# Kernel tuning notes

Measured on AMD Instinct MI355X. Metric: run time of the kernel, lower is better.

## Reference

```python
import jax, jax.numpy as jnp
import numpy as np

NUM_CLASSES = 15
ANGLE_BINS = 90
ANGLE_SCALE = float(np.pi / 2 / ANGLE_BINS)
TOPK, A_ALPHA, A_BETA = 13, 1.0, 6.0
F_ALPHA, F_GAMMA = 0.75, 2.0
W_CLS, W_BOX, W_ANGLE = 1.0, 2.5, 0.05
EPS = 1e-9


def make_anchors(img=1024, strides=(8, 16, 32)):
    pts, strs = [], []
    for s in strides:
        n = img // s
        xs = (np.arange(n, dtype=np.float32) + 0.5) * s  # pixel-space centers
        X, Y = np.meshgrid(xs, xs)
        pts.append(np.stack([X.ravel(), Y.ravel()], -1))
        strs.append(np.full((n * n, 1), s, np.float32))
    return np.concatenate(pts)[None].astype(np.float32), np.concatenate(strs)[None]


def decode_boxes(anchor_points, reg_dist, raw_angles, stride_tensor, angle_proj):
    # DFL-style angle: softmax over bins projected onto angle values
    angle = jnp.einsum('bna,a->bn', jax.nn.softmax(raw_angles, axis=-1), angle_proj)  # [B,N]
    lt, rb = reg_dist[..., :2], reg_dist[..., 2:]
    off = (rb - lt) * 0.5
    c, s = jnp.cos(angle), jnp.sin(angle)
    ox = off[..., 0] * c - off[..., 1] * s
    oy = off[..., 0] * s + off[..., 1] * c
    xy = jnp.stack([ox, oy], -1) * stride_tensor + anchor_points
    wh = (lt + rb) * stride_tensor
    return jnp.concatenate([xy, wh, angle[..., None]], -1)  # [B,N,5]


def _cov(b):
    # rotated box -> 2D Gaussian covariance terms
    w, h, a = b[..., 2], b[..., 3], b[..., 4]
    A, B = w * w / 12.0, h * h / 12.0
    c, s = jnp.cos(a), jnp.sin(a)
    return A * c * c + B * s * s, A * s * s + B * c * c, (A - B) * c * s


def probiou_hd(b1, b2, eps=1e-3):
    # Hellinger distance between Gaussian boxes; probiou similarity = 1 - hd
    x1, y1, x2, y2 = b1[..., 0], b1[..., 1], b2[..., 0], b2[..., 1]
    a1, bb1, c1 = _cov(b1)
    a2, bb2, c2 = _cov(b2)
    denom = (a1 + a2) * (bb1 + bb2) - (c1 + c2) ** 2 + eps
    t1 = ((a1 + a2) * (y1 - y2) ** 2 + (bb1 + bb2) * (x1 - x2) ** 2) / denom * 0.25
    t2 = ((c1 + c2) * (x2 - x1) * (y1 - y2)) / denom * 0.5
    det1 = jnp.maximum(a1 * bb1 - c1 * c1, 0.0)
    det2 = jnp.maximum(a2 * bb2 - c2 * c2, 0.0)
    t3 = 0.5 * jnp.log(denom / (4.0 * jnp.sqrt(det1 * det2) + eps) + eps)
    bd = jnp.clip(t1 + t2 + t3, eps, 100.0)
    return jnp.sqrt(1.0 - jnp.exp(-bd) + 1e-7)


def assign(pred_scores, pred_boxes, anchor_points, gt_labels, gt_boxes, pad_gt_mask, bg_index):
    B, M = gt_labels.shape[:2]
    N = pred_boxes.shape[1]
    C = pred_scores.shape[-1]
    lbl = gt_labels[..., 0]  # [B,M]
    # rotated ProbIoU between every GT and every pred box: [B,M,N]
    ious = jnp.maximum(1.0 - probiou_hd(gt_boxes[:, :, None, :], pred_boxes[:, None, :, :]), 0.0)
    # gather pred class score at each gt's label: [B,M,N]
    scores = jnp.einsum('bnc,bmc->bmn', pred_scores, jax.nn.one_hot(lbl, C, dtype=pred_scores.dtype))
    align = (scores ** A_ALPHA) * (ious ** A_BETA)
    # anchor-center inside rotated GT box
    dx = anchor_points[:, None, :, 0] - gt_boxes[:, :, None, 0]
    dy = anchor_points[:, None, :, 1] - gt_boxes[:, :, None, 1]
    ca, sa = jnp.cos(gt_boxes[:, :, None, 4]), jnp.sin(gt_boxes[:, :, None, 4])
    xr = dx * ca + dy * sa
    yr = -dx * sa + dy * ca
    in_gt = (jnp.abs(xr) < gt_boxes[:, :, None, 2] * 0.5) & (jnp.abs(yr) < gt_boxes[:, :, None, 3] * 0.5)
    mask_cand = in_gt.astype(align.dtype) * pad_gt_mask  # [B,M,N]
    # top-k alignment candidates per GT
    topv, topi = jax.lax.top_k(align * mask_cand, TOPK)
    valid = (topv > EPS).astype(align.dtype)
    bi = jnp.arange(B)[:, None, None]
    mi = jnp.arange(M)[None, :, None]
    topk_mask = jnp.zeros((B, M, N), align.dtype).at[bi, mi, topi].max(valid)
    mask_pos = topk_mask * mask_cand
    # resolve anchors matched to multiple GTs via max IoU
    fg = mask_pos.sum(1)  # [B,N]
    is_max_iou = jax.nn.one_hot(jnp.argmax(ious, axis=1), M, axis=1, dtype=align.dtype)
    mask_pos = jnp.where(fg[:, None, :] > 1, is_max_iou, mask_pos)
    fg = mask_pos.sum(1)
    tgt_idx = jnp.argmax(mask_pos, axis=1)  # [B,N]
    fg_mask = fg > 0
    assigned_labels = jnp.where(fg_mask, jnp.take_along_axis(lbl, tgt_idx, axis=1), bg_index)
    assigned_boxes = jnp.take_along_axis(gt_boxes, tgt_idx[..., None], axis=1)  # [B,N,5]
    # normalize alignment metric by per-GT max IoU / max align
    align_pos = align * mask_pos
    max_align = align_pos.max(-1, keepdims=True)
    max_iou = (ious * mask_pos).max(-1, keepdims=True)
    norm_align = (align_pos * max_iou / (max_align + EPS)).max(1)  # [B,N]
    onehot = jax.nn.one_hot(assigned_labels, C + 1, dtype=align.dtype)[..., :C]
    assigned_scores = onehot * norm_align[..., None]
    return assigned_labels, assigned_boxes, assigned_scores


def _bce_logits(x, t):
    return jnp.maximum(x, 0.0) - x * t + jnp.log1p(jnp.exp(-jnp.abs(x)))


def compute_loss(cls_logits, reg_dist, raw_angles, gt_labels, gt_boxes, valid_mask,
                 anchor_points, stride_tensor, angle_proj):
    C = NUM_CLASSES
    decoded = decode_boxes(anchor_points, reg_dist, raw_angles, stride_tensor, angle_proj)
    cls_scores = jax.nn.sigmoid(cls_logits)
    al, ab, ascore = assign(jax.lax.stop_gradient(cls_scores), jax.lax.stop_gradient(decoded),
                            anchor_points, gt_labels, gt_boxes, valid_mask, C)
    score_sum = jnp.maximum(ascore.sum(), 1.0)
    # varifocal classification loss
    onehot = jax.nn.one_hot(al, C + 1, dtype=cls_logits.dtype)[..., :C]
    fw = F_ALPHA * (cls_scores ** F_GAMMA) * (1.0 - onehot) + ascore * onehot
    loss_cls = (_bce_logits(cls_logits, ascore) * fw).sum() / score_sum
    # ProbIoU box loss over positives, weighted by assigned scores
    posf = (al != C).astype(cls_logits.dtype)
    iou_loss = probiou_hd(decoded, ab)  # [B,N]
    bw = ascore.sum(-1)
    loss_box = (iou_loss * bw * posf).sum() / score_sum
    # DFL angle loss: interpolate CE between neighboring bins
    t = jnp.clip(ab[..., 4] / ANGLE_SCALE, 0.0, ANGLE_BINS - 0.01)
    li = t.astype(jnp.int32)
    ri = jnp.minimum(li + 1, ANGLE_BINS)
    lw = ri.astype(t.dtype) - t
    rw = 1.0 - lw
    logp = jax.nn.log_softmax(raw_angles, axis=-1)
    ce_l = -jnp.take_along_axis(logp, li[..., None], axis=-1)[..., 0]
    ce_r = -jnp.take_along_axis(logp, ri[..., None], axis=-1)[..., 0]
    npos = jnp.maximum(posf.sum(), 1.0)
    loss_angle = ((ce_l * lw + ce_r * rw) * posf).sum() / npos
    total = W_CLS * loss_cls + W_BOX * loss_box + W_ANGLE * loss_angle
    return total, loss_cls, loss_box, loss_angle


def setup_inputs() -> dict:
    key = jax.random.key(0)
    ks = jax.random.split(key, 8)
    B, M, C, AB = 16, 64, NUM_CLASSES, ANGLE_BINS
    anchor_np, stride_np = make_anchors()
    N = anchor_np.shape[1]  # 21504
    cls_logits = jax.random.normal(ks[0], (B, N, C), jnp.float32) - 2.0
    reg_dist = jax.random.uniform(ks[1], (B, N, 4), jnp.float32, 0.0, 6.0)
    raw_angles = jax.random.normal(ks[2], (B, N, AB + 1), jnp.float32)
    gt_labels = jax.random.randint(ks[3], (B, M, 1), 0, C)
    cxy = jax.random.uniform(ks[4], (B, M, 2), jnp.float32, 32.0, 992.0)
    wh = jax.random.uniform(ks[5], (B, M, 2), jnp.float32, 16.0, 160.0)
    ang = jax.random.uniform(ks[6], (B, M, 1), jnp.float32, 0.0, float(np.pi / 2) - 1e-3)
    gt_boxes = jnp.concatenate([cxy, wh, ang], -1)
    valid_mask = (jax.random.uniform(ks[7], (B, M, 1)) < 0.8).astype(jnp.float32)
    angle_proj = jnp.arange(AB + 1, dtype=jnp.float32) * ANGLE_SCALE
    return dict(cls_logits=cls_logits, reg_dist=reg_dist, raw_angles=raw_angles,
                gt_labels=gt_labels, gt_boxes=gt_boxes, valid_mask=valid_mask,
                anchor_points=jnp.asarray(anchor_np), stride_tensor=jnp.asarray(stride_np),
                angle_proj=angle_proj)


def reference(cls_logits, reg_dist, raw_angles, gt_labels, gt_boxes, valid_mask,
              anchor_points, stride_tensor, angle_proj):
    return compute_loss(cls_logits, reg_dist, raw_angles, gt_labels, gt_boxes, valid_mask,
                        anchor_points, stride_tensor, angle_proj)
```

## Files before the change

kernel.cpp:

```cpp
#include <hip/hip_runtime.h>

#define TK 13
#define EPSA 1e-9f
#define MMAX 128
#define CMAX 1024
#define DROWS 64
#define A1F 91
#define CF 15

__device__ __forceinline__ float frcp(float x) { return __builtin_amdgcn_rcpf(x); }

__device__ __forceinline__ void anchor_of(int n, float& ax, float& ay, float& st) {
    if (n < 16384)      { st = 8.0f;  ax = ((n & 127) + 0.5f) * 8.0f;  ay = ((n >> 7) + 0.5f) * 8.0f; }
    else if (n < 20480) { int q = n - 16384; st = 16.0f; ax = ((q & 63) + 0.5f) * 16.0f; ay = ((q >> 6) + 0.5f) * 16.0f; }
    else                { int q = n - 20480; st = 32.0f; ax = ((q & 31) + 0.5f) * 32.0f; ay = ((q >> 5) + 0.5f) * 32.0f; }
}

__device__ __forceinline__ float hd_cov(float x1, float y1, float a1, float b1, float c1, float sd1,
                                        float x2, float y2, float a2, float b2, float c2, float sd2) {
    float sa = a1 + a2, sb = b1 + b2, sc = c1 + c2;
    float denom = sa * sb - sc * sc + 1e-3f;
    float inv = frcp(denom);
    float dy = y1 - y2, dx = x1 - x2;
    float t1 = (sa * dy * dy + sb * dx * dx) * inv * 0.25f;
    float t2 = sc * (x2 - x1) * (y1 - y2) * inv * 0.5f;
    float t3 = 0.5f * __logf(denom * frcp(4.0f * sd1 * sd2 + 1e-3f) + 1e-3f);
    float bd = fminf(fmaxf(t1 + t2 + t3, 1e-3f), 100.0f);
    return sqrtf(1.0f - __expf(-bd) + 1e-7f);
}

__device__ __forceinline__ void cov5(float w, float h, float ang,
                                     float& ca, float& cb, float& cc, float& sd) {
    float A = w * w * (1.0f / 12.0f), B = h * h * (1.0f / 12.0f);
    float c = __cosf(ang), s = __sinf(ang);
    ca = A * c * c + B * s * s;
    cb = A * s * s + B * c * c;
    cc = (A - B) * c * s;
    sd = sqrtf(fmaxf(ca * cb - cc * cc, 0.0f));
}

__global__ __launch_bounds__(256) void k_decode(
    const float* __restrict__ reg, const float* __restrict__ rawang,
    float4* __restrict__ dec4, float2* __restrict__ dcs,
    float* __restrict__ lse_out,
    int* __restrict__ zbase, int zwords,
    int BN, int N) {
    __shared__ float srow[DROWS * A1F];
    int tid = threadIdx.x;
    int gstride = gridDim.x * 256;
    for (int z = blockIdx.x * 256 + tid; z < zwords; z += gstride) zbase[z] = 0;
    int r0 = blockIdx.x * DROWS;
    if (r0 >= BN) return;
    if (r0 + DROWS <= BN) {
        const float4* g4 = (const float4*)(rawang + (size_t)r0 * A1F);
        float4* s4 = (float4*)srow;
#pragma unroll
        for (int k = 0; k < (DROWS * A1F) / 4 / 256 + 1; ++k) {
            int j = tid + k * 256;
            if (j < (DROWS * A1F) / 4) s4[j] = g4[j];
        }
    } else {
        const float* gs = rawang + (size_t)r0 * A1F;
        int lim = (BN - r0) * A1F;
        for (int k = tid; k < lim; k += 256) srow[k] = gs[k];
    }
    __syncthreads();
    int row = tid >> 2, sub = tid & 3;
    int idx = r0 + row;
    if (idx >= BN) return;
    int j0 = sub * 23;
    int jn = (sub == 3) ? 22 : 23;
    const float* rp = srow + row * A1F + j0;
    float s = 0.0f, num = 0.0f;
#pragma unroll
    for (int i = 0; i < 23; ++i) {
        if (i < jn) {
            float e = __expf(rp[i]);
            s += e;
            num = fmaf(e, (float)(j0 + i), num);
        }
    }
    s += __shfl_xor(s, 1); num += __shfl_xor(num, 1);
    s += __shfl_xor(s, 2); num += __shfl_xor(num, 2);
    if (sub == 0) {
        float ang = 0.017453292519943295f * num * frcp(s);
        float lse = __logf(s);
        int n = idx % N;
        float4 rg = *(const float4*)(reg + (size_t)idx * 4);
        float l0 = rg.x, l1 = rg.y, rr0 = rg.z, rr1 = rg.w;
        float offx = (rr0 - l0) * 0.5f, offy = (rr1 - l1) * 0.5f;
        float c = __cosf(ang), sn = __sinf(ang);
        float ox = offx * c - offy * sn, oy = offx * sn + offy * c;
        float ax, ay, st;
        anchor_of(n, ax, ay, st);
        float x = ox * st + ax;
        float y = oy * st + ay;
        float w = (l0 + rr0) * st, hh = (l1 + rr1) * st;
        float ca, cb, cc, sd;
        cov5(w, hh, ang, ca, cb, cc, sd);
        dec4[idx] = make_float4(x, y, ca, cb);
        dcs[idx] = make_float2(cc, sd);
        lse_out[idx] = lse;
    }
}

__global__ __launch_bounds__(256) void k_topk(
    const float4* __restrict__ dec4, const float2* __restrict__ dcs,
    const float* __restrict__ cls,
    const float* __restrict__ gtb, const int* __restrict__ gtl,
    const float* __restrict__ vmask,
    int* __restrict__ fg, int* __restrict__ tgtc,
    int B, int M, int N, int C) {
    int m = blockIdx.x, b = blockIdx.y;
    if (vmask[b * M + m] == 0.0f) return;
    const float* g = gtb + (size_t)(b * M + m) * 5;
    float gx = g[0], gy = g[1], gw = g[2], gh = g[3], gang = g[4];
    float gca, gcb, gcc, gsd;
    cov5(gw, gh, gang, gca, gcb, gcc, gsd);
    float cA = __cosf(gang), sA = __sinf(gang);
    int lbl = gtl[b * M + m];
    float hw = 0.5f * gw, hh2 = 0.5f * gh;
    float hx = fabsf(hw * cA) + fabsf(hh2 * sA);
    float hy = fabsf(hw * sA) + fabsf(hh2 * cA);
    int tid = threadIdx.x;
    size_t bN = (size_t)b * N;

    __shared__ int cnt;
    __shared__ float cval[CMAX];
    __shared__ int cidx[CMAX];
    if (tid == 0) cnt = 0;
    __syncthreads();

    const int off_[3] = {0, 16384, 20480};
    const int gs_[3]  = {128, 64, 32};
    const float st_[3] = {8.0f, 16.0f, 32.0f};
#pragma unroll
    for (int lv = 0; lv < 3; ++lv) {
        float st = st_[lv];
        int gs = gs_[lv], off = off_[lv];
        float ist = frcp(st);
        int i0 = (int)floorf((gx - hx) * ist - 0.5f);
        int i1 = (int)ceilf((gx + hx) * ist - 0.5f);
        int j0 = (int)floorf((gy - hy) * ist - 0.5f);
        int j1 = (int)ceilf((gy + hy) * ist - 0.5f);
        i0 = max(i0, 0); j0 = max(j0, 0);
        i1 = min(i1, gs - 1); j1 = min(j1, gs - 1);
        int w = i1 - i0 + 1, hgt = j1 - j0 + 1;
        int tot = (w > 0 && hgt > 0) ? w * hgt : 0;
        for (int t = tid; t < tot; t += 256) {
            int ii = i0 + t % w, jj = j0 + t / w;
            float ax = (ii + 0.5f) * st, ay = (jj + 0.5f) * st;
            float dx = ax - gx, dy = ay - gy;
            float xr = dx * cA + dy * sA;
            float yr = -dx * sA + dy * cA;
            if (fabsf(xr) < hw && fabsf(yr) < hh2) {
                int n = off + jj * gs + ii;
                float4 dd = dec4[bN + n];
                float2 cs = dcs[bN + n];
                float hd = hd_cov(gx, gy, gca, gcb, gcc, gsd,
                                  dd.x, dd.y, dd.z, dd.w, cs.x, cs.y);
                float iou = fmaxf(1.0f - hd, 0.0f);
                float xl = cls[(bN + n) * C + lbl];
                float p = frcp(1.0f + __expf(-xl));
                float i2 = iou * iou;
                float v = p * (i2 * i2 * i2);
                if (v > EPSA) {
                    int pos = atomicAdd(&cnt, 1);
                    if (pos < CMAX) { cval[pos] = v; cidx[pos] = n; }
                }
            }
        }
    }
    __syncthreads();

    int total = min(cnt, CMAX);
    int rounds = min(total, TK);
    if (tid < 64) {
        for (int r = 0; r < rounds; ++r) {
            float bv = -1.0f; int bn = 0x7fffffff; int bp = -1;
            for (int j = tid; j < total; j += 64) {
                float v = cval[j];
                int nn = cidx[j];
                if (v > bv || (v == bv && nn < bn)) { bv = v; bn = nn; bp = j; }
            }
            for (int o = 32; o; o >>= 1) {
                float ov = __shfl_xor(bv, o);
                int on = __shfl_xor(bn, o);
                int op = __shfl_xor(bp, o);
                if (ov > bv || (ov == bv && on < bn)) { bv = ov; bn = on; bp = op; }
            }
            if (tid == 0) {
                atomicAdd(&fg[bN + bn], 1);
                atomicMax(&tgtc[bN + bn], m);
            }
            if ((bp & 63) == tid) cval[bp] = -2.0f;
        }
    }
}

__global__ __launch_bounds__(256) void k_select(
    const float4* __restrict__ dec4, const float2* __restrict__ dcs,
    const float* __restrict__ cls,
    const float* __restrict__ gtb, const int* __restrict__ gtl,
    const int* __restrict__ fg, const int* __restrict__ tgtc,
    int* __restrict__ tgt_out, float* __restrict__ align_out,
    unsigned int* __restrict__ max_align, unsigned int* __restrict__ max_iou,
    int B, int M, int N, int C) {
    __shared__ float gx[MMAX], gy[MMAX], ga[MMAX], gb[MMAX], gc[MMAX], gsd[MMAX];
    __shared__ int glb[MMAX];
    int b = blockIdx.y;
    int tid = threadIdx.x;
    if (tid < M) {
        const float* g = gtb + (size_t)(b * M + tid) * 5;
        float ca, cb, cc, sd;
        cov5(g[2], g[3], g[4], ca, cb, cc, sd);
        gx[tid] = g[0]; gy[tid] = g[1]; ga[tid] = ca; gb[tid] = cb; gc[tid] = cc; gsd[tid] = sd;
        glb[tid] = gtl[b * M + tid];
    }
    __syncthreads();
    int n = blockIdx.x * 256 + tid;
    if (n >= N) return;
    size_t bN = (size_t)b * N;
    int f = fg[bN + n];
    if (f == 0) return;
    float4 dd = dec4[bN + n];
    float2 cs = dcs[bN + n];
    float px = dd.x, py = dd.y, pa = dd.z, pb = dd.w, pc = cs.x, psd = cs.y;
    int mstar;
    float ioustar;
    if (f == 1) {
        mstar = tgtc[bN + n];
        float hd = hd_cov(gx[mstar], gy[mstar], ga[mstar], gb[mstar], gc[mstar], gsd[mstar],
                          px, py, pa, pb, pc, psd);
        ioustar = fmaxf(1.0f - hd, 0.0f);
    } else {
        float best = -1.0f; int bm = 0;
        for (int mm = 0; mm < M; mm++) {
            float hd = hd_cov(gx[mm], gy[mm], ga[mm], gb[mm], gc[mm], gsd[mm],
                              px, py, pa, pb, pc, psd);
            float iou = fmaxf(1.0f - hd, 0.0f);
            if (iou > best) { best = iou; bm = mm; }
        }
        mstar = bm; ioustar = best;
    }
    int lbl = glb[mstar];
    float xl = cls[(bN + n) * C + lbl];
    float p = frcp(1.0f + __expf(-xl));
    float i2 = ioustar * ioustar;
    float al = p * (i2 * i2 * i2);
    tgt_out[bN + n] = mstar + 1;
    align_out[bN + n] = al;
    atomicMax(&max_align[b * M + mstar], __float_as_uint(al));
    atomicMax(&max_iou[b * M + mstar], __float_as_uint(ioustar));
}

__global__ __launch_bounds__(256) void k_loss(
    const float4* __restrict__ dec4, const float2* __restrict__ dcs,
    const float* __restrict__ cls,
    const float* __restrict__ rawang, const float* __restrict__ lse_in,
    const float* __restrict__ gtb, const int* __restrict__ gtl,
    const int* __restrict__ tgt_in, const float* __restrict__ align_in,
    const float* __restrict__ max_align, const float* __restrict__ max_iou,
    float* __restrict__ pblk,
    int B, int M, int N, int C, int A1) {
    __shared__ float gx[MMAX], gy[MMAX], ga[MMAX], gb[MMAX], gc[MMAX], gsd[MMAX], gan[MMAX];
    __shared__ int glb[MMAX];
    int b = blockIdx.y;
    int tid = threadIdx.x;
    if (tid < M) {
        const float* g = gtb + (size_t)(b * M + tid) * 5;
        float ca, cb, cc, sd;
        cov5(g[2], g[3], g[4], ca, cb, cc, sd);
        gx[tid] = g[0]; gy[tid] = g[1]; ga[tid] = ca; gb[tid] = cb; gc[tid] = cc; gsd[tid] = sd;
        gan[tid] = g[4];
        glb[tid] = gtl[b * M + tid];
    }
    __syncthreads();
    int n = blockIdx.x * 256 + tid;
    float s_cls = 0.0f, s_box = 0.0f, s_ang = 0.0f, s_asc = 0.0f, s_pos = 0.0f;
    if (n < N) {
        size_t bN = (size_t)b * N;
        int tg1 = tgt_in[bN + n];
        int lbl = -1;
        float norm = 0.0f;
        if (tg1 > 0) {
            int tg = tg1 - 1;
            lbl = glb[tg];
            norm = align_in[bN + n] * max_iou[b * M + tg] * frcp(max_align[b * M + tg] + 1e-9f);
            float4 dd = dec4[bN + n];
            float2 cs = dcs[bN + n];
            float hd = hd_cov(dd.x, dd.y, dd.z, dd.w, cs.x, cs.y,
                              gx[tg], gy[tg], ga[tg], gb[tg], gc[tg], gsd[tg]);
            s_box = hd * norm;
            s_asc = norm;
            s_pos = 1.0f;
            float tt = fminf(fmaxf(gan[tg] * 57.29577951308232f, 0.0f), 89.99f);
            int li = (int)tt;
            int ri = min(li + 1, 90);
            float lw = (float)ri - tt;
            float rw = 1.0f - lw;
            float lse = lse_in[bN + n];
            const float* arow = rawang + (bN + n) * A1;
            float ce_l = lse - arow[li];
            float ce_r = lse - arow[ri];
            s_ang = ce_l * lw + ce_r * rw;
        }
        const float* xrow = cls + (bN + n) * CF;
#pragma unroll
        for (int c = 0; c < CF; c++) {
            float x = xrow[c];
            float e = __expf(-fabsf(x));
            float inv = frcp(1.0f + e);
            float p = (x >= 0.0f) ? inv : 1.0f - inv;
            bool pos = (c == lbl);
            float t = pos ? norm : 0.0f;
            float fw = pos ? norm : 0.75f * p * p;
            float bce = fmaxf(x, 0.0f) - x * t - __logf(inv);
            s_cls += bce * fw;
        }
    }
    for (int off = 32; off; off >>= 1) {
        s_cls += __shfl_xor(s_cls, off);
        s_box += __shfl_xor(s_box, off);
        s_ang += __shfl_xor(s_ang, off);
        s_asc += __shfl_xor(s_asc, off);
        s_pos += __shfl_xor(s_pos, off);
    }
    __shared__ float red[4][5];
    int w = tid >> 6, lane = tid & 63;
    if (lane == 0) {
        red[w][0] = s_cls; red[w][1] = s_box; red[w][2] = s_ang;
        red[w][3] = s_asc; red[w][4] = s_pos;
    }
    __syncthreads();
    if (tid == 0) {
        int bid = blockIdx.y * gridDim.x + blockIdx.x;
        float* p = pblk + (size_t)bid * 5;
        p[0] = red[0][0] + red[1][0] + red[2][0] + red[3][0];
        p[1] = red[0][1] + red[1][1] + red[2][1] + red[3][1];
        p[2] = red[0][2] + red[1][2] + red[2][2] + red[3][2];
        p[3] = red[0][3] + red[1][3] + red[2][3] + red[3][3];
        p[4] = red[0][4] + red[1][4] + red[2][4] + red[3][4];
    }
}

__global__ __launch_bounds__(256) void k_final(
    const float* __restrict__ pblk, int nblk, float* __restrict__ out) {
    int tid = threadIdx.x;
    float a0 = 0, a1 = 0, a2 = 0, a3 = 0, a4 = 0;
    for (int j = tid; j < nblk; j += 256) {
        const float* p = pblk + (size_t)j * 5;
        a0 += p[0]; a1 += p[1]; a2 += p[2]; a3 += p[3]; a4 += p[4];
    }
    for (int off = 32; off; off >>= 1) {
        a0 += __shfl_xor(a0, off);
        a1 += __shfl_xor(a1, off);
        a2 += __shfl_xor(a2, off);
        a3 += __shfl_xor(a3, off);
        a4 += __shfl_xor(a4, off);
    }
    __shared__ float red[4][5];
    int w = tid >> 6, lane = tid & 63;
    if (lane == 0) { red[w][0] = a0; red[w][1] = a1; red[w][2] = a2; red[w][3] = a3; red[w][4] = a4; }
    __syncthreads();
    if (tid == 0) {
        float s0 = 0, s1 = 0, s2 = 0, s3 = 0, s4 = 0;
        for (int i = 0; i < 4; i++) {
            s0 += red[i][0]; s1 += red[i][1]; s2 += red[i][2]; s3 += red[i][3]; s4 += red[i][4];
        }
        float ssum = fmaxf(s3, 1.0f);
        float npos = fmaxf(s4, 1.0f);
        float lc = s0 / ssum;
        float lb = s1 / ssum;
        float la = s2 / npos;
        out[0] = 1.0f * lc + 2.5f * lb + 0.05f * la;
        out[1] = lc;
        out[2] = lb;
        out[3] = la;
    }
}

extern "C" void kernel_launch(void* const* d_in, const int* in_sizes, int n_in,
                              void* d_out, int out_size, void* d_ws, size_t ws_size,
                              hipStream_t stream) {
    const float* cls    = (const float*)d_in[0];
    const float* reg    = (const float*)d_in[1];
    const float* rawang = (const float*)d_in[2];
    const int*   gtl    = (const int*)d_in[3];
    const float* gtb    = (const float*)d_in[4];
    const float* vmask  = (const float*)d_in[5];

    int N  = in_sizes[6] / 2;
    int B  = in_sizes[1] / (4 * N);
    int BN = B * N;
    int C  = in_sizes[0] / BN;
    int M  = in_sizes[3] / B;
    int A1 = in_sizes[2] / BN;

    float* ws = (float*)d_ws;
    float4* dec4    = (float4*)ws;
    float2* dcs     = (float2*)(dec4 + BN);
    float*  lse     = (float*)(dcs + BN);
    int*    fg      = (int*)(lse + BN);
    int*    tgtc    = fg + BN;
    int*    tgt     = tgtc + BN;
    float*  align_at = (float*)(tgt + BN);
    unsigned int* mxal = (unsigned int*)(align_at + BN);
    unsigned int* mxio = mxal + B * M;
    float*  pblk    = (float*)(mxio + B * M);

    int zwords = BN * 4 + B * M * 2;

    k_decode<<<dim3((BN + DROWS - 1) / DROWS), dim3(256), 0, stream>>>(
        reg, rawang, dec4, dcs, lse, fg, zwords, BN, N);
    k_topk<<<dim3(M, B), dim3(256), 0, stream>>>(
        dec4, dcs, cls, gtb, gtl, vmask, fg, tgtc, B, M, N, C);
    int gx = (N + 255) / 256;
    dim3 g45(gx, B);
    k_select<<<g45, dim3(256), 0, stream>>>(
        dec4, dcs, cls, gtb, gtl, fg, tgtc, tgt, align_at, mxal, mxio, B, M, N, C);
    k_loss<<<g45, dim3(256), 0, stream>>>(
        dec4, dcs, cls, rawang, lse, gtb, gtl, tgt, align_at,
        (const float*)mxal, (const float*)mxio, pblk, B, M, N, C, A1);
    k_final<<<1, 256, 0, stream>>>(pblk, gx * B, (float*)d_out);
}
```

Before: 295.9 us.

## Fuse select and loss kernels via per-GT sums of normalized loss terms

Merges the select and loss kernels by rewriting the normalized positive terms algebraically. The per-anchor loss factors as r*align, with r = max_iou/max_align per ground truth, so per-GT atomic sums of align, hd*align, BCE*align and x*align^2 are accumulated and scaled by r in the final kernel. The negative focal loss over all anchors and classes moves into the decode kernel, and a correction term is subtracted for positive anchors. This removes one full pass over the anchors and the per-anchor target and align arrays. In exchange it adds float atomicAdd contention on per-GT accumulators, a non-deterministic summation order, and extra class-logit reads in decode.

```diff
diff --git a/kernel.cpp b/kernel.cpp
--- a/kernel.cpp
+++ b/kernel.cpp
@@ -9,12 +9,6 @@
 #define CF 15
 
 __device__ __forceinline__ float frcp(float x) { return __builtin_amdgcn_rcpf(x); }
-
-__device__ __forceinline__ void anchor_of(int n, float& ax, float& ay, float& st) {
-    if (n < 16384)      { st = 8.0f;  ax = ((n & 127) + 0.5f) * 8.0f;  ay = ((n >> 7) + 0.5f) * 8.0f; }
-    else if (n < 20480) { int q = n - 16384; st = 16.0f; ax = ((q & 63) + 0.5f) * 16.0f; ay = ((q >> 6) + 0.5f) * 16.0f; }
-    else                { int q = n - 20480; st = 32.0f; ax = ((q & 31) + 0.5f) * 32.0f; ay = ((q >> 5) + 0.5f) * 32.0f; }
-}
 
 __device__ __forceinline__ float hd_cov(float x1, float y1, float a1, float b1, float c1, float sd1,
                                         float x2, float y2, float a2, float b2, float c2, float sd2) {
@@ -39,10 +33,17 @@
     sd = sqrtf(fmaxf(ca * cb - cc * cc, 0.0f));
 }
 
+__device__ __forceinline__ void anchor_of(int n, float& ax, float& ay, float& st) {
+    if (n < 16384)      { st = 8.0f;  ax = ((n & 127) + 0.5f) * 8.0f;  ay = ((n >> 7) + 0.5f) * 8.0f; }
+    else if (n < 20480) { int q = n - 16384; st = 16.0f; ax = ((q & 63) + 0.5f) * 16.0f; ay = ((q >> 6) + 0.5f) * 16.0f; }
+    else                { int q = n - 20480; st = 32.0f; ax = ((q & 31) + 0.5f) * 32.0f; ay = ((q >> 5) + 0.5f) * 32.0f; }
+}
+
 __global__ __launch_bounds__(256) void k_decode(
     const float* __restrict__ reg, const float* __restrict__ rawang,
+    const float* __restrict__ cls,
     float4* __restrict__ dec4, float2* __restrict__ dcs,
-    float* __restrict__ lse_out,
+    float* __restrict__ lse_out, float* __restrict__ pblkA,
     int* __restrict__ zbase, int zwords,
     int BN, int N) {
     __shared__ float srow[DROWS * A1F];
@@ -50,7 +51,6 @@
     int gstride = gridDim.x * 256;
     for (int z = blockIdx.x * 256 + tid; z < zwords; z += gstride) zbase[z] = 0;
     int r0 = blockIdx.x * DROWS;
-    if (r0 >= BN) return;
     if (r0 + DROWS <= BN) {
         const float4* g4 = (const float4*)(rawang + (size_t)r0 * A1F);
         float4* s4 = (float4*)srow;
@@ -59,7 +59,7 @@
             int j = tid + k * 256;
             if (j < (DROWS * A1F) / 4) s4[j] = g4[j];
         }
-    } else {
+    } else if (r0 < BN) {
         const float* gs = rawang + (size_t)r0 * A1F;
         int lim = (BN - r0) * A1F;
         for (int k = tid; k < lim; k += 256) srow[k] = gs[k];
@@ -67,22 +67,38 @@
     __syncthreads();
     int row = tid >> 2, sub = tid & 3;
     int idx = r0 + row;
-    if (idx >= BN) return;
-    int j0 = sub * 23;
-    int jn = (sub == 3) ? 22 : 23;
-    const float* rp = srow + row * A1F + j0;
+    bool live = idx < BN;
+    float negacc = 0.0f;
     float s = 0.0f, num = 0.0f;
+    if (live) {
+        int j0 = sub * 23;
+        int jn = (sub == 3) ? 22 : 23;
+        const float* rp = srow + row * A1F + j0;
 #pragma unroll
-    for (int i = 0; i < 23; ++i) {
-        if (i < jn) {
-            float e = __expf(rp[i]);
-            s += e;
-            num = fmaf(e, (float)(j0 + i), num);
+        for (int i = 0; i < 23; ++i) {
+            if (i < jn) {
+                float e = __expf(rp[i]);
+                s += e;
+                num = fmaf(e, (float)(j0 + i), num);
+            }
+        }
+        const float* xrow = cls + (size_t)idx * CF;
+#pragma unroll
+        for (int i = 0; i < 4; ++i) {
+            int c = sub * 4 + i;
+            if (c < CF) {
+                float x = xrow[c];
+                float e = __expf(-fabsf(x));
+                float inv = frcp(1.0f + e);
+                float p = (x >= 0.0f) ? inv : 1.0f - inv;
+                float A = fmaxf(x, 0.0f) - __logf(inv);
+                negacc += 0.75f * p * p * A;
+            }
         }
     }
     s += __shfl_xor(s, 1); num += __shfl_xor(num, 1);
     s += __shfl_xor(s, 2); num += __shfl_xor(num, 2);
-    if (sub == 0) {
+    if (live && sub == 0) {
         float ang = 0.017453292519943295f * num * frcp(s);
         float lse = __logf(s);
         int n = idx % N;
@@ -102,6 +118,11 @@
         dcs[idx] = make_float2(cc, sd);
         lse_out[idx] = lse;
     }
+    for (int o = 32; o; o >>= 1) negacc += __shfl_xor(negacc, o);
+    __shared__ float wred[4];
+    if ((tid & 63) == 0) wred[tid >> 6] = negacc;
+    __syncthreads();
+    if (tid == 0) pblkA[blockIdx.x] = wred[0] + wred[1] + wred[2] + wred[3];
 }
 
 __global__ __launch_bounds__(256) void k_topk(
@@ -201,67 +222,13 @@
 __global__ __launch_bounds__(256) void k_select(
     const float4* __restrict__ dec4, const float2* __restrict__ dcs,
     const float* __restrict__ cls,
+    const float* __restrict__ rawang, const float* __restrict__ lse_in,
     const float* __restrict__ gtb, const int* __restrict__ gtl,
     const int* __restrict__ fg, const int* __restrict__ tgtc,
-    int* __restrict__ tgt_out, float* __restrict__ align_out,
-    unsigned int* __restrict__ max_align, unsigned int* __restrict__ max_iou,
-    int B, int M, int N, int C) {
-    __shared__ float gx[MMAX], gy[MMAX], ga[MMAX], gb[MMAX], gc[MMAX], gsd[MMAX];
-    __shared__ int glb[MMAX];
-    int b = blockIdx.y;
-    int tid = threadIdx.x;
-    if (tid < M) {
-        const float* g = gtb + (size_t)(b * M + tid) * 5;
-        float ca, cb, cc, sd;
-        cov5(g[2], g[3], g[4], ca, cb, cc, sd);
-        gx[tid] = g[0]; gy[tid] = g[1]; ga[tid] = ca; gb[tid] = cb; gc[tid] = cc; gsd[tid] = sd;
-        glb[tid] = gtl[b * M + tid];
-    }
-    __syncthreads();
-    int n = blockIdx.x * 256 + tid;
-    if (n >= N) return;
-    size_t bN = (size_t)b * N;
-    int f = fg[bN + n];
-    if (f == 0) return;
-    float4 dd = dec4[bN + n];
-    float2 cs = dcs[bN + n];
-    float px = dd.x, py = dd.y, pa = dd.z, pb = dd.w, pc = cs.x, psd = cs.y;
-    int mstar;
-    float ioustar;
-    if (f == 1) {
-        mstar = tgtc[bN + n];
-        float hd = hd_cov(gx[mstar], gy[mstar], ga[mstar], gb[mstar], gc[mstar], gsd[mstar],
-                          px, py, pa, pb, pc, psd);
-        ioustar = fmaxf(1.0f - hd, 0.0f);
-    } else {
-        float best = -1.0f; int bm = 0;
-        for (int mm = 0; mm < M; mm++) {
-            float hd = hd_cov(gx[mm], gy[mm], ga[mm], gb[mm], gc[mm], gsd[mm],
-                              px, py, pa, pb, pc, psd);
-            float iou = fmaxf(1.0f - hd, 0.0f);
-            if (iou > best) { best = iou; bm = mm; }
-        }
-        mstar = bm; ioustar = best;
-    }
-    int lbl = glb[mstar];
-    float xl = cls[(bN + n) * C + lbl];
-    float p = frcp(1.0f + __expf(-xl));
-    float i2 = ioustar * ioustar;
-    float al = p * (i2 * i2 * i2);
-    tgt_out[bN + n] = mstar + 1;
-    align_out[bN + n] = al;
-    atomicMax(&max_align[b * M + mstar], __float_as_uint(al));
-    atomicMax(&max_iou[b * M + mstar], __float_as_uint(ioustar));
-}
-
-__global__ __launch_bounds__(256) void k_loss(
-    const float4* __restrict__ dec4, const float2* __restrict__ dcs,
-    const float* __restrict__ cls,
-    const float* __restrict__ rawang, const float* __restrict__ lse_in,
-    const float* __restrict__ gtb, const int* __restrict__ gtl,
-    const int* __restrict__ tgt_in, const float* __restrict__ align_in,
-    const float* __restrict__ max_align, const float* __restrict__ max_iou,
-    float* __restrict__ pblk,
+    unsigned int* __restrict__ mxal, unsigned int* __restrict__ mxio,
+    float* __restrict__ gtSa, float* __restrict__ gtSb,
+    float* __restrict__ gtSc1, float* __restrict__ gtSc2,
+    float* __restrict__ pblkB,
     int B, int M, int N, int C, int A1) {
     __shared__ float gx[MMAX], gy[MMAX], ga[MMAX], gb[MMAX], gc[MMAX], gsd[MMAX], gan[MMAX];
     __shared__ int glb[MMAX];
@@ -277,102 +244,126 @@
     }
     __syncthreads();
     int n = blockIdx.x * 256 + tid;
-    float s_cls = 0.0f, s_box = 0.0f, s_ang = 0.0f, s_asc = 0.0f, s_pos = 0.0f;
+    size_t bN = (size_t)b * N;
+    float s_ang = 0.0f, s_fix = 0.0f, s_pos = 0.0f;
     if (n < N) {
-        size_t bN = (size_t)b * N;
-        int tg1 = tgt_in[bN + n];
-        int lbl = -1;
-        float norm = 0.0f;
-        if (tg1 > 0) {
-            int tg = tg1 - 1;
-            lbl = glb[tg];
-            norm = align_in[bN + n] * max_iou[b * M + tg] * frcp(max_align[b * M + tg] + 1e-9f);
+        int f = fg[bN + n];
+        if (f > 0) {
             float4 dd = dec4[bN + n];
             float2 cs = dcs[bN + n];
-            float hd = hd_cov(dd.x, dd.y, dd.z, dd.w, cs.x, cs.y,
-                              gx[tg], gy[tg], ga[tg], gb[tg], gc[tg], gsd[tg]);
-            s_box = hd * norm;
-            s_asc = norm;
+            float px = dd.x, py = dd.y, pa = dd.z, pb = dd.w, pc = cs.x, psd = cs.y;
+            int mstar;
+            float ioustar;
+            if (f == 1) {
+                mstar = tgtc[bN + n];
+                float hd = hd_cov(gx[mstar], gy[mstar], ga[mstar], gb[mstar], gc[mstar], gsd[mstar],
+                                  px, py, pa, pb, pc, psd);
+                ioustar = fmaxf(1.0f - hd, 0.0f);
+            } else {
+                float best = -1.0f; int bm = 0;
+                for (int mm = 0; mm < M; mm++) {
+                    float hd = hd_cov(gx[mm], gy[mm], ga[mm], gb[mm], gc[mm], gsd[mm],
+                                      px, py, pa, pb, pc, psd);
+                    float iou = fmaxf(1.0f - hd, 0.0f);
+                    if (iou > best) { best = iou; bm = mm; }
+                }
+                mstar = bm; ioustar = best;
+            }
+            float hd = 1.0f - ioustar;
+            int lbl = glb[mstar];
+            float x = cls[(bN + n) * C + lbl];
+            float e = __expf(-fabsf(x));
+            float inv = frcp(1.0f + e);
+            float p = (x >= 0.0f) ? inv : 1.0f - inv;
+            float A = fmaxf(x, 0.0f) - __logf(inv);
+            float i2 = ioustar * ioustar;
+            float al = p * (i2 * i2 * i2);
+            int g = b * M + mstar;
+            atomicMax(&mxal[g], __float_as_uint(al));
+            atomicMax(&mxio[g], __float_as_uint(ioustar));
+            atomicAdd(&gtSa[g], al);
+            atomicAdd(&gtSb[g], hd * al);
+            atomicAdd(&gtSc1[g], A * al);
+            atomicAdd(&gtSc2[g], x * al * al);
+            s_fix = 0.75f * p * p * A;
             s_pos = 1.0f;
-            float tt = fminf(fmaxf(gan[tg] * 57.29577951308232f, 0.0f), 89.99f);
+            float tt = fminf(fmaxf(gan[mstar] * 57.29577951308232f, 0.0f), 89.99f);
             int li = (int)tt;
             int ri = min(li + 1, 90);
             float lw = (float)ri - tt;
             float rw = 1.0f - lw;
             float lse = lse_in[bN + n];
             const float* arow = rawang + (bN + n) * A1;
-            float ce_l = lse - arow[li];
-            float ce_r = lse - arow[ri];
-            s_ang = ce_l * lw + ce_r * rw;
-        }
-        const float* xrow = cls + (bN + n) * CF;
-#pragma unroll
-        for (int c = 0; c < CF; c++) {
-            float x = xrow[c];
-            float e = __expf(-fabsf(x));
-            float inv = frcp(1.0f + e);
-            float p = (x >= 0.0f) ? inv : 1.0f - inv;
-            bool pos = (c == lbl);
-            float t = pos ? norm : 0.0f;
-            float fw = pos ? norm : 0.75f * p * p;
-            float bce = fmaxf(x, 0.0f) - x * t - __logf(inv);
-            s_cls += bce * fw;
-        }
-    }
-    for (int off = 32; off; off >>= 1) {
-        s_cls += __shfl_xor(s_cls, off);
-        s_box += __shfl_xor(s_box, off);
-        s_ang += __shfl_xor(s_ang, off);
-        s_asc += __shfl_xor(s_asc, off);
-        s_pos += __shfl_xor(s_pos, off);
-    }
-    __shared__ float red[4][5];
+            s_ang = (lse - arow[li]) * lw + (lse - arow[ri]) * rw;
+        }
+    }
+    for (int o = 32; o; o >>= 1) {
+        s_ang += __shfl_xor(s_ang, o);
+        s_fix += __shfl_xor(s_fix, o);
+        s_pos += __shfl_xor(s_pos, o);
+    }
+    __shared__ float red[4][3];
     int w = tid >> 6, lane = tid & 63;
-    if (lane == 0) {
-        red[w][0] = s_cls; red[w][1] = s_box; red[w][2] = s_ang;
-        red[w][3] = s_asc; red[w][4] = s_pos;
-    }
+    if (lane == 0) { red[w][0] = s_ang; red[w][1] = s_fix; red[w][2] = s_pos; }
     __syncthreads();
     if (tid == 0) {
         int bid = blockIdx.y * gridDim.x + blockIdx.x;
-        float* p = pblk + (size_t)bid * 5;
+        float* p = pblkB + (size_t)bid * 3;
         p[0] = red[0][0] + red[1][0] + red[2][0] + red[3][0];
         p[1] = red[0][1] + red[1][1] + red[2][1] + red[3][1];
         p[2] = red[0][2] + red[1][2] + red[2][2] + red[3][2];
-        p[3] = red[0][3] + red[1][3] + red[2][3] + red[3][3];
-        p[4] = red[0][4] + red[1][4] + red[2][4] + red[3][4];
     }
 }
 
 __global__ __launch_bounds__(256) void k_final(
-    const float* __restrict__ pblk, int nblk, float* __restrict__ out) {
+    const float* __restrict__ pblkA, int nA,
+    const float* __restrict__ pblkB, int nB,
+    const unsigned int* __restrict__ mxal, const unsigned int* __restrict__ mxio,
+    const float* __restrict__ gtSa, const float* __restrict__ gtSb,
+    const float* __restrict__ gtSc1, const float* __restrict__ gtSc2,
+    int BM, float* __restrict__ out) {
     int tid = threadIdx.x;
-    float a0 = 0, a1 = 0, a2 = 0, a3 = 0, a4 = 0;
-    for (int j = tid; j < nblk; j += 256) {
-        const float* p = pblk + (size_t)j * 5;
-        a0 += p[0]; a1 += p[1]; a2 += p[2]; a3 += p[3]; a4 += p[4];
-    }
-    for (int off = 32; off; off >>= 1) {
-        a0 += __shfl_xor(a0, off);
-        a1 += __shfl_xor(a1, off);
-        a2 += __shfl_xor(a2, off);
-        a3 += __shfl_xor(a3, off);
-        a4 += __shfl_xor(a4, off);
-    }
-    __shared__ float red[4][5];
+    float neg = 0.0f;
+    for (int j = tid; j < nA; j += 256) neg += pblkA[j];
+    float ang = 0.0f, fix = 0.0f, pos = 0.0f;
+    for (int j = tid; j < nB; j += 256) {
+        const float* p = pblkB + (size_t)j * 3;
+        ang += p[0]; fix += p[1]; pos += p[2];
+    }
+    float cpos = 0.0f, bx = 0.0f, asc = 0.0f;
+    for (int g = tid; g < BM; g += 256) {
+        float ma = __uint_as_float(mxal[g]);
+        float mi = __uint_as_float(mxio[g]);
+        float r = mi * frcp(ma + 1e-9f);
+        cpos += r * gtSc1[g] - r * r * gtSc2[g];
+        bx += r * gtSb[g];
+        asc += r * gtSa[g];
+    }
+    for (int o = 32; o; o >>= 1) {
+        neg += __shfl_xor(neg, o);
+        ang += __shfl_xor(ang, o);
+        fix += __shfl_xor(fix, o);
+        pos += __shfl_xor(pos, o);
+        cpos += __shfl_xor(cpos, o);
+        bx += __shfl_xor(bx, o);
+        asc += __shfl_xor(asc, o);
+    }
+    __shared__ float red[4][7];
     int w = tid >> 6, lane = tid & 63;
-    if (lane == 0) { red[w][0] = a0; red[w][1] = a1; red[w][2] = a2; red[w][3] = a3; red[w][4] = a4; }
+    if (lane == 0) {
+        red[w][0] = neg; red[w][1] = ang; red[w][2] = fix; red[w][3] = pos;
+        red[w][4] = cpos; red[w][5] = bx; red[w][6] = asc;
+    }
     __syncthreads();
     if (tid == 0) {
-        float s0 = 0, s1 = 0, s2 = 0, s3 = 0, s4 = 0;
-        for (int i = 0; i < 4; i++) {
-            s0 += red[i][0]; s1 += red[i][1]; s2 += red[i][2]; s3 += red[i][3]; s4 += red[i][4];
-        }
-        float ssum = fmaxf(s3, 1.0f);
-        float npos = fmaxf(s4, 1.0f);
-        float lc = s0 / ssum;
-        float lb = s1 / ssum;
-        float la = s2 / npos;
+        float s[7] = {0, 0, 0, 0, 0, 0, 0};
+        for (int i = 0; i < 4; i++)
+            for (int k = 0; k < 7; k++) s[k] += red[i][k];
+        float ssum = fmaxf(s[6], 1.0f);
+        float npos = fmaxf(s[3], 1.0f);
+        float lc = (s[0] - s[2] + s[4]) / ssum;
+        float lb = s[5] / ssum;
+        float la = s[1] / npos;
         out[0] = 1.0f * lc + 2.5f * lb + 0.05f * la;
         out[1] = lc;
         out[2] = lb;
@@ -396,6 +387,7 @@
     int C  = in_sizes[0] / BN;
     int M  = in_sizes[3] / B;
     int A1 = in_sizes[2] / BN;
+    int BM = B * M;
 
     float* ws = (float*)d_ws;
     float4* dec4    = (float4*)ws;
@@ -403,24 +395,28 @@
     float*  lse     = (float*)(dcs + BN);
     int*    fg      = (int*)(lse + BN);
     int*    tgtc    = fg + BN;
-    int*    tgt     = tgtc + BN;
-    float*  align_at = (float*)(tgt + BN);
-    unsigned int* mxal = (unsigned int*)(align_at + BN);
-    unsigned int* mxio = mxal + B * M;
-    float*  pblk    = (float*)(mxio + B * M);
-
-    int zwords = BN * 4 + B * M * 2;
-
-    k_decode<<<dim3((BN + DROWS - 1) / DROWS), dim3(256), 0, stream>>>(
-        reg, rawang, dec4, dcs, lse, fg, zwords, BN, N);
+    unsigned int* mxal = (unsigned int*)(tgtc + BN);
+    unsigned int* mxio = mxal + BM;
+    float*  gtSa    = (float*)(mxio + BM);
+    float*  gtSb    = gtSa + BM;
+    float*  gtSc1   = gtSb + BM;
+    float*  gtSc2   = gtSc1 + BM;
+    float*  pblkA   = gtSc2 + BM;
+    int nblkA = (BN + DROWS - 1) / DROWS;
+    float*  pblkB   = pblkA + nblkA;
+
+    int zwords = BN * 2 + BM * 6;
+
+    k_decode<<<dim3(nblkA), dim3(256), 0, stream>>>(
+        reg, rawang, cls, dec4, dcs, lse, pblkA, fg, zwords, BN, N);
     k_topk<<<dim3(M, B), dim3(256), 0, stream>>>(
         dec4, dcs, cls, gtb, gtl, vmask, fg, tgtc, B, M, N, C);
     int gx = (N + 255) / 256;
-    dim3 g45(gx, B);
-    k_select<<<g45, dim3(256), 0, stream>>>(
-        dec4, dcs, cls, gtb, gtl, fg, tgtc, tgt, align_at, mxal, mxio, B, M, N, C);
-    k_loss<<<g45, dim3(256), 0, stream>>>(
-        dec4, dcs, cls, rawang, lse, gtb, gtl, tgt, align_at,
-        (const float*)mxal, (const float*)mxio, pblk, B, M, N, C, A1);
-    k_final<<<1, 256, 0, stream>>>(pblk, gx * B, (float*)d_out);
-}
+    dim3 g3(gx, B);
+    k_select<<<g3, dim3(256), 0, stream>>>(
+        dec4, dcs, cls, rawang, lse, gtb, gtl, fg, tgtc,
+        mxal, mxio, gtSa, gtSb, gtSc1, gtSc2, pblkB, B, M, N, C, A1);
+    k_final<<<1, 256, 0, stream>>>(
+        pblkA, nblkA, pblkB, gx * B, mxal, mxio, gtSa, gtSb, gtSc1, gtSc2,
+        BM, (float*)d_out);
+}
```

Result: faster. 285.5 us (-3.5%).
